# Optimization experiments

Measured on AMD Instinct MI355X. Metric: run time of the kernel, lower is better.

Reference implementation:

```python
import jax, jax.numpy as jnp
import numpy as np

# Config constants (mirror EnergyConfig)
MIN_CARD = 26.0
CARD_PEN = 25.0
PLANE_W = 1.0
FACET_W = 8.0
RANK_EPS = 1e-6
BOUND_W = 4.0
SUP_W = 1.0
ACT_W = 1.0
INACT_W = 0.35
MARGIN = 0.05
PROB_POW = 1.0
PLANE_TOPK = 128
ACTIVE_TOPK = 64

N_POINTS, DIM, BATCH = 65536, 8, 256


def _topk_filter(w, k):
    # Keep only the top-k entries per row, zero elsewhere (scatter of gathered values).
    if k <= 0 or k >= w.shape[-1]:
        return w
    vals, idx = jax.lax.top_k(w, k)
    rows = jnp.arange(w.shape[0])[:, None]
    return jnp.zeros_like(w).at[rows, idx].set(vals)


def setup_inputs() -> dict:
    key = jax.random.key(0)
    k1, k2 = jax.random.split(key)
    probabilities = jax.random.uniform(k1, (BATCH, N_POINTS), dtype=jnp.float32)
    points = jax.random.normal(k2, (N_POINTS, DIM), dtype=jnp.float32)
    return {"probabilities": probabilities, "points": points}


def reference(probabilities, points):
    prob = jnp.clip(probabilities, 1e-5, 1.0 - 1e-5)  # (B,N)

    # ---- weighted plane statistics (weighted PCA) ----
    pw = _topk_filter(prob, PLANE_TOPK)                       # (B,N)
    wsum = jnp.clip(pw.sum(-1), 1e-6)                          # (B,)
    mean = (pw @ points) / wsum[:, None]                       # (B,D)
    pp = points[:, :, None] * points[:, None, :]               # (N,D,D), small since D=8
    second_moment = jnp.einsum('bn,nij->bij', pw, pp) / wsum[:, None, None]
    cov = second_moment - mean[:, :, None] * mean[:, None, :]  # (B,D,D)
    cov = 0.5 * (cov + cov.swapaxes(1, 2))
    eigvals, eigvecs = jnp.linalg.eigh(cov)                    # ascending
    plane_term = eigvals[:, 0]
    second_eig = eigvals[:, 1]
    facet_term = plane_term / (second_eig + RANK_EPS)
    normal = eigvecs[:, :, 0]                                  # (B,D) smallest-eig direction

    # ---- dual-orientation boundary terms ----
    proj = points @ normal.T                                   # (N,B)
    active_w = _topk_filter(prob ** PROB_POW, ACTIVE_TOPK)     # (B,N)
    active_norm = jnp.clip(active_w.sum(-1), 1e-6)
    inactive_w = 1.0 - prob
    inactive_norm = jnp.clip(inactive_w.sum(-1), 1e-6)

    def orientation_boundary(p):
        # p: (N,B) oriented projections
        offset = -p.max(axis=0)                                # (B,)
        signed = p + offset[None, :]                           # (N,B), max is 0
        sb = signed.T                                          # (B,N)
        active_res = sb * sb                                   # quadratic active loss
        active = (active_w * active_res).sum(-1) / active_norm
        slack = jax.nn.relu(MARGIN + sb)
        inactive = (inactive_w * slack * slack).sum(-1) / inactive_norm
        support = jax.nn.relu(signed.max(axis=0)) ** 2
        return SUP_W * support + ACT_W * active + INACT_W * inactive

    b_pos = orientation_boundary(proj)
    b_neg = orientation_boundary(-proj)
    boundary = jnp.where(b_pos <= b_neg, b_pos, b_neg)

    # ---- cardinality penalty ----
    cardinality = prob.sum(-1)
    deficit = jax.nn.relu(MIN_CARD - cardinality)
    card_term = CARD_PEN * deficit * deficit

    total = PLANE_W * plane_term + FACET_W * facet_term + BOUND_W * boundary + card_term
    return total
```

## Files before the change

kernel.cpp:

```cpp
#include <hip/hip_runtime.h>
#include <cstdint>
#include <cstddef>

constexpr int NPTS   = 65536;
constexpr int B      = 256;
constexpr int CHUNKS = 8;
constexpr int CHUNK  = NPTS / CHUNKS;
constexpr int CCAP   = 160;
constexpr int NBLK   = B * CHUNKS;
constexpr int NEARCAP = 256;

constexpr size_t WSO_CBUF    = 0;
constexpr size_t WSO_NEAR    = WSO_CBUF + (size_t)NBLK * CCAP * 2;
constexpr size_t WSO_NEARCNT = WSO_NEAR + (size_t)2 * B * NEARCAP * 2;
constexpr size_t WSO_PSUM    = WSO_NEARCNT + 2 * B;
constexpr size_t WSO_CCNT    = WSO_PSUM + NBLK;
constexpr size_t WSO_PLANE   = WSO_CCNT + NBLK;
constexpr size_t WSO_FACET   = WSO_PLANE + B;
constexpr size_t WSO_NRM     = WSO_FACET + B;
constexpr size_t WSO_SUMP    = WSO_NRM + (size_t)B * 8;
constexpr size_t WSO_ANORM   = WSO_SUMP + B;
constexpr size_t WSO_T64V    = WSO_ANORM + B;
constexpr size_t WSO_T64I    = WSO_T64V + (size_t)B * 64;
constexpr size_t WSO_PMAXP   = WSO_T64I + (size_t)B * 64;
constexpr size_t WSO_PMAXN   = WSO_PMAXP + B;

constexpr int PPB = 64;
constexpr int NPB = NPTS / PPB;
constexpr size_t WSO_PART = WSO_CBUF;

__device__ __forceinline__ float clipp(float x) {
    return fminf(fmaxf(x, 1e-5f), 0.99999f);
}
__device__ __forceinline__ unsigned f2mono(float f) {
    unsigned u = __float_as_uint(f);
    return (u & 0x80000000u) ? ~u : (u | 0x80000000u);
}
__device__ __forceinline__ float mono2f(unsigned e) {
    return __uint_as_float((e & 0x80000000u) ? (e ^ 0x80000000u) : ~e);
}
__device__ __forceinline__ int cand_bin(float v) {
    int b = (int)((v - 0.99f) * 102400.0f);
    return min(max(b, 0), 1023);
}
__device__ __forceinline__ float dot8(float4 a, float4 b, const float* n) {
    float d = a.x * n[0];
    d = fmaf(a.y, n[1], d); d = fmaf(a.z, n[2], d); d = fmaf(a.w, n[3], d);
    d = fmaf(b.x, n[4], d); d = fmaf(b.y, n[5], d); d = fmaf(b.z, n[6], d);
    d = fmaf(b.w, n[7], d);
    return d;
}
__device__ __forceinline__ float dot8v(float4 a, float4 b, float4 n0, float4 n1) {
    float d = a.x * n0.x;
    d = fmaf(a.y, n0.y, d); d = fmaf(a.z, n0.z, d); d = fmaf(a.w, n0.w, d);
    d = fmaf(b.x, n1.x, d); d = fmaf(b.y, n1.y, d); d = fmaf(b.z, n1.z, d);
    d = fmaf(b.w, n1.w, d);
    return d;
}

__global__ __launch_bounds__(256) void kA_stream(
    const float* __restrict__ prob, float* __restrict__ ws)
{
    __shared__ float wred[4];
    __shared__ int lcnt;
    const int tid   = threadIdx.x;
    const int row   = blockIdx.x >> 3;
    const int chunk = blockIdx.x & 7;
    if (tid == 0) lcnt = 0;
    __syncthreads();

    unsigned long long* cb = (unsigned long long*)ws + (size_t)blockIdx.x * CCAP;
    const float4* p4 = (const float4*)(prob + (size_t)row * NPTS + (size_t)chunk * CHUNK);

    float4 v[8];
    #pragma unroll
    for (int i = 0; i < 8; i++) v[i] = p4[i * 256 + tid];

    float lsum = 0.f;
    #pragma unroll
    for (int i = 0; i < 8; i++) {
        float c0 = clipp(v[i].x), c1 = clipp(v[i].y), c2 = clipp(v[i].z), c3 = clipp(v[i].w);
        lsum += (c0 + c1) + (c2 + c3);
        float mx = fmaxf(fmaxf(c0, c1), fmaxf(c2, c3));
        if (mx >= 0.99f) {
            int bi = chunk * CHUNK + (i * 256 + tid) * 4;
            float c4[4] = {c0, c1, c2, c3};
            #pragma unroll
            for (int j = 0; j < 4; j++) {
                if (c4[j] >= 0.99f) {
                    int p_ = atomicAdd(&lcnt, 1);
                    if (p_ < CCAP)
                        cb[p_] = (((unsigned long long)__float_as_uint(c4[j])) << 32)
                               | (unsigned)~(bi + j);
                }
            }
        }
    }
    #pragma unroll
    for (int off = 32; off; off >>= 1) lsum += __shfl_down(lsum, off);
    if ((tid & 63) == 0) wred[tid >> 6] = lsum;
    __syncthreads();
    if (tid == 0) {
        ws[WSO_PSUM + blockIdx.x] = (wred[0] + wred[1]) + (wred[2] + wred[3]);
        ((int*)ws)[WSO_CCNT + blockIdx.x] = min(lcnt, CCAP);
    }
}

constexpr int CSLOTS = CHUNKS * CCAP;
constexpr int GITER  = CSLOTS / 256;
__global__ __launch_bounds__(256) void kB_select(
    const float* __restrict__ points, float* __restrict__ ws)
{
    __shared__ unsigned long long cand[CSLOTS];
    __shared__ unsigned long long comp[256];
    __shared__ int   hist[1024];
    __shared__ int   counts_s[CHUNKS];
    __shared__ int   ccnt_s, bt_s;
    __shared__ float sw[128];
    __shared__ float pc[128][9];
    __shared__ float sred[44][4];
    __shared__ float slotm[44];
    __shared__ float wpart[2];
    __shared__ float covm[64];

    const int row = blockIdx.x;
    const int tid = threadIdx.x;

    if (tid < CHUNKS) counts_s[tid] = ((const int*)ws)[WSO_CCNT + row * CHUNKS + tid];
    if (tid == 0) { ccnt_s = 0; bt_s = 0; }
    #pragma unroll
    for (int k = 0; k < 4; k++) hist[tid * 4 + k] = 0;
    __syncthreads();

    const unsigned long long* cb = (const unsigned long long*)ws;
    #pragma unroll
    for (int r = 0; r < GITER; r++) {
        int s = r * 256 + tid;
        int c = s / CCAP, t = s - c * CCAP;
        unsigned long long k = 0ull;
        if (t < counts_s[c]) {
            k = cb[(size_t)(row * CHUNKS + c) * CCAP + t];
            atomicAdd(&hist[cand_bin(__uint_as_float((unsigned)(k >> 32)))], 1);
        }
        cand[s] = k;
    }
    __syncthreads();

    if (tid < 64) {
        int h[16]; int g = 0;
        #pragma unroll
        for (int k = 0; k < 16; k++) { h[k] = hist[tid * 16 + k]; g += h[k]; }
        int s = g;
        #pragma unroll
        for (int off = 1; off < 64; off <<= 1) {
            int o = __shfl_down(s, off);
            if (tid + off < 64) s += o;
        }
        int Snext = __shfl_down(s, 1);
        if (tid == 63) Snext = 0;
        if (s >= 128 && Snext < 128) {
            int acc = Snext, bt = tid * 16;
            #pragma unroll
            for (int k = 15; k >= 0; k--) {
                acc += h[k];
                if (acc >= 128) { bt = tid * 16 + k; break; }
            }
            bt_s = bt;
        }
    }
    __syncthreads();

    const int bt = bt_s;
    #pragma unroll
    for (int r = 0; r < GITER; r++) {
        unsigned long long k = cand[r * 256 + tid];
        if (k && cand_bin(__uint_as_float((unsigned)(k >> 32))) >= bt) {
            int p_ = atomicAdd(&ccnt_s, 1);
            if (p_ < 256) comp[p_] = k;
        }
    }
    __syncthreads();
    const int m = min(ccnt_s, 256);

    if (tid < 128) {
        sw[tid] = 0.f;
        #pragma unroll
        for (int j = 0; j < 9; j++) pc[tid][j] = (j == 8) ? 1.f : 0.f;
    }
    if (tid < 64) {
        ws[WSO_T64V + (size_t)row * 64 + tid] = 0.f;
        ((int*)ws)[WSO_T64I + (size_t)row * 64 + tid] = 0;
    }
    unsigned long long ki = (tid < m) ? comp[tid] : 0ull;
    int rank = 0;
    for (int j = 0; j < m; j++) rank += (comp[j] > ki) ? 1 : 0;
    __syncthreads();

    if (tid < m && rank < 128) {
        float v = __uint_as_float((unsigned)(ki >> 32));
        unsigned idx = ~(unsigned)(ki & 0xFFFFFFFFu);
        sw[rank] = v;
        const float4* pt = (const float4*)(points + (size_t)idx * 8);
        float4 q0 = pt[0], q1 = pt[1];
        pc[rank][0] = q0.x; pc[rank][1] = q0.y; pc[rank][2] = q0.z; pc[rank][3] = q0.w;
        pc[rank][4] = q1.x; pc[rank][5] = q1.y; pc[rank][6] = q1.z; pc[rank][7] = q1.w;
        if (rank < 64) {
            ws[WSO_T64V + (size_t)row * 64 + rank] = v;
            ((int*)ws)[WSO_T64I + (size_t)row * 64 + rank] = (int)idx;
        }
    }
    __syncthreads();

    if (tid < 128) {
        float ww = sw[tid];
        #pragma unroll
        for (int off = 32; off; off >>= 1) ww += __shfl_down(ww, off);
        if ((tid & 63) == 0) wpart[tid >> 6] = ww;
    }
    if (tid < 176) {
        int s = tid >> 2, part = tid & 3;
        int i_, j_;
        if (s < 36) {
            int rem = s; i_ = 0;
            while (rem >= 8 - i_) { rem -= 8 - i_; i_++; }
            j_ = i_ + rem;
        } else { i_ = s - 36; j_ = 8; }
        float acc = 0.f;
        for (int k = part * 32; k < part * 32 + 32; k++)
            acc += sw[k] * pc[k][i_] * pc[k][j_];
        sred[s][part] = acc;
    }
    __syncthreads();
    if (tid < 44) slotm[tid] = (sred[tid][0] + sred[tid][1]) + (sred[tid][2] + sred[tid][3]);
    __syncthreads();

    if (tid < 64) {
        float w128 = fmaxf(wpart[0] + wpart[1], 1e-6f);
        int i_ = tid >> 3, j_ = tid & 7;
        int a_ = min(i_, j_), b_ = max(i_, j_);
        int s3 = 8 * a_ - (a_ * (a_ - 1)) / 2 + (b_ - a_);
        covm[tid] = slotm[s3] / w128 - (slotm[36 + i_] / w128) * (slotm[36 + j_] / w128);
    }
    __syncthreads();

    if (tid == 64) {
        ws[WSO_ANORM + row] = fmaxf(wpart[0], 1e-6f);
        float s = 0.f;
        for (int c = 0; c < CHUNKS; c++) s += ws[WSO_PSUM + row * CHUNKS + c];
        ws[WSO_SUMP + row] = s;
        ((unsigned*)ws)[WSO_PMAXP + row] = 0u;
        ((unsigned*)ws)[WSO_PMAXN + row] = 0u;
        ((int*)ws)[WSO_NEARCNT + row * 2 + 0] = 0;
        ((int*)ws)[WSO_NEARCNT + row * 2 + 1] = 0;
    }

    if (tid < 64) {
        const int i = tid >> 3, j = tid & 7;
        float a = covm[tid];
        float v = (i == j) ? 1.f : 0.f;
        const unsigned PR[7] = {023456701u, 001234567u, 050712346u, 034067125u,
                                012305674u, 067120453u, 045671032u};
        #pragma unroll 1
        for (int sweep = 0; sweep < 6; sweep++) {
            #pragma unroll
            for (int r = 0; r < 7; r++) {
                const unsigned pk = PR[r];
                const int rp = (pk >> (3 * i)) & 7;
                const int cp = (pk >> (3 * j)) & 7;
                const int pr = min(i, rp), qr = max(i, rp);
                float app = __shfl(a, pr * 9);
                float aqq = __shfl(a, qr * 9);
                float apq = __shfl(a, pr * 8 + qr);
                float tau = 0.5f * (aqq - app);
                float den = fabsf(tau) + sqrtf(fmaf(tau, tau, apq * apq));
                float t = __fdividef(apq, den + 1e-38f);
                t = (tau < 0.f) ? -t : t;
                float cr = rsqrtf(fmaf(t, t, 1.f));
                float sr = t * cr;
                float cc = __shfl(cr, j * 9);
                float sc = __shfl(sr, j * 9);
                float oth = __shfl(a, rp * 8 + j);
                a = fmaf((i < rp) ? -sr : sr, oth, cr * a);
                float oth2 = __shfl(a, i * 8 + cp);
                a = fmaf((j < cp) ? -sc : sc, oth2, cc * a);
                float ov = __shfl(v, i * 8 + cp);
                v = fmaf((j < cp) ? -sc : sc, ov, cc * v);
            }
        }
        float d[8];
        #pragma unroll
        for (int k = 0; k < 8; k++) d[k] = __shfl(a, k * 9);
        float e0 = d[0]; int i0 = 0;
        #pragma unroll
        for (int k = 1; k < 8; k++) if (d[k] < e0) { e0 = d[k]; i0 = k; }
        float e1 = 3.4e38f;
        #pragma unroll
        for (int k = 0; k < 8; k++) if (k != i0 && d[k] < e1) e1 = d[k];
        if (tid == 0) {
            ws[WSO_PLANE + row] = e0;
            ws[WSO_FACET + row] = e0 / (e1 + 1e-6f);
        }
        if (j == i0) ws[WSO_NRM + (size_t)row * 8 + i] = v;
    }
}

__global__ __launch_bounds__(256) void k3a_max(
    const float* __restrict__ points, float* __restrict__ ws)
{
    const int t  = threadIdx.x;
    const int pb = blockIdx.x;
    const float4* nv = (const float4*)(ws + WSO_NRM);
    float4 n0 = nv[t * 2], n1 = nv[t * 2 + 1];
    const float4* pq = (const float4*)points + (size_t)pb * (PPB * 2);
    float mp = -3.4e38f, mn = -3.4e38f;
    #pragma unroll 8
    for (int i = 0; i < PPB; i++) {
        float4 a = pq[2 * i], b = pq[2 * i + 1];
        float d = dot8v(a, b, n0, n1);
        mp = fmaxf(mp, d);
        mn = fmaxf(mn, -d);
    }
    float* part = ws + WSO_PART + (size_t)pb * 512;
    part[t * 2]     = mp;
    part[t * 2 + 1] = mn;
}

__global__ __launch_bounds__(256) void k3r_reduce(float* __restrict__ ws)
{
    const int tg = blockIdx.x * 256 + threadIdx.x;
    const int rs = tg & 511;
    const int g  = tg >> 9;
    const float* part = ws + WSO_PART;
    float m = -3.4e38f;
    #pragma unroll 8
    for (int i = 0; i < NPB / 8; i++)
        m = fmaxf(m, part[(size_t)(g * (NPB / 8) + i) * 512 + rs]);
    unsigned* wsu = (unsigned*)ws;
    atomicMax(&wsu[((rs & 1) ? WSO_PMAXN : WSO_PMAXP) + (rs >> 1)], f2mono(m));
}

__global__ __launch_bounds__(256) void k3b_near(
    const float* __restrict__ points, float* __restrict__ ws)
{
    const int t  = threadIdx.x;
    const int pb = blockIdx.x;
    const unsigned* wsu = (const unsigned*)ws;
    const float4* nv = (const float4*)(ws + WSO_NRM);
    float4 n0 = nv[t * 2], n1 = nv[t * 2 + 1];
    const float thp = mono2f(wsu[WSO_PMAXP + t]) - 0.05f;
    const float thn = mono2f(wsu[WSO_PMAXN + t]) - 0.05f;
    const float4* pq = (const float4*)points + (size_t)pb * (PPB * 2);
    int* ncnt = (int*)ws + WSO_NEARCNT;
    unsigned long long* nbuf = (unsigned long long*)ws + WSO_NEAR / 2;
    #pragma unroll 4
    for (int i = 0; i < PPB; i++) {
        float4 a = pq[2 * i], b = pq[2 * i + 1];
        float d = dot8v(a, b, n0, n1);
        int nidx = pb * PPB + i;
        if (d >= thp) {
            int p_ = atomicAdd(&ncnt[t * 2 + 0], 1);
            if (p_ < NEARCAP)
                nbuf[(size_t)(t * 2 + 0) * NEARCAP + p_] =
                    (((unsigned long long)__float_as_uint(d)) << 32) | (unsigned)nidx;
        }
        if (-d >= thn) {
            int p_ = atomicAdd(&ncnt[t * 2 + 1], 1);
            if (p_ < NEARCAP)
                nbuf[(size_t)(t * 2 + 1) * NEARCAP + p_] =
                    (((unsigned long long)__float_as_uint(-d)) << 32) | (unsigned)nidx;
        }
    }
}

__global__ __launch_bounds__(64) void k3cd_final(
    const float* __restrict__ points, const float* __restrict__ prob,
    const float* __restrict__ ws, float* __restrict__ out)
{
    const int row = blockIdx.x;
    const int t   = threadIdx.x;
    const unsigned* wsu = (const unsigned*)ws;
    __shared__ float nl[8];
    if (t < 8) nl[t] = ws[WSO_NRM + (size_t)row * 8 + t];
    __syncthreads();

    const float pmaxp = mono2f(wsu[WSO_PMAXP + row]);
    const float pmaxn = mono2f(wsu[WSO_PMAXN + row]);

    float w   = ws[WSO_T64V + (size_t)row * 64 + t];
    int   idx = ((const int*)ws)[WSO_T64I + (size_t)row * 64 + t];
    const float4* pt = (const float4*)(points + (size_t)idx * 8);
    float4 q0 = pt[0], q1 = pt[1];
    float d = dot8(q0, q1, nl);
    float sp = d - pmaxp, sn = -d - pmaxn;
    float ap = w * sp * sp;
    float an = w * sn * sn;

    const int* ncnt = (const int*)ws + WSO_NEARCNT;
    const unsigned long long* nbuf = (const unsigned long long*)ws + WSO_NEAR / 2;
    float ip = 0.f, in_ = 0.f;
    int cp = min(ncnt[row * 2 + 0], NEARCAP);
    int cn = min(ncnt[row * 2 + 1], NEARCAP);
    for (int i = t; i < cp; i += 64) {
        unsigned long long e = nbuf[(size_t)(row * 2 + 0) * NEARCAP + i];
        float dv = __uint_as_float((unsigned)(e >> 32));
        float tp = 0.05f + (dv - pmaxp);
        if (tp > 0.f) {
            float w2 = 1.0f - clipp(prob[(size_t)row * NPTS + (unsigned)(e & 0xFFFFFFFFu)]);
            ip = fmaf(w2 * tp, tp, ip);
        }
    }
    for (int i = t; i < cn; i += 64) {
        unsigned long long e = nbuf[(size_t)(row * 2 + 1) * NEARCAP + i];
        float dv = __uint_as_float((unsigned)(e >> 32));
        float tn = 0.05f + (dv - pmaxn);
        if (tn > 0.f) {
            float w2 = 1.0f - clipp(prob[(size_t)row * NPTS + (unsigned)(e & 0xFFFFFFFFu)]);
            in_ = fmaf(w2 * tn, tn, in_);
        }
    }
    #pragma unroll
    for (int off = 32; off; off >>= 1) {
        ap  += __shfl_down(ap, off);
        an  += __shfl_down(an, off);
        ip  += __shfl_down(ip, off);
        in_ += __shfl_down(in_, off);
    }
    if (t == 0) {
        float anorm = ws[WSO_ANORM + row];
        float sump  = ws[WSO_SUMP + row];
        float inorm = fmaxf((float)NPTS - sump, 1e-6f);
        float bp = (ap / anorm) + 0.35f * (ip / inorm);
        float bn = (an / anorm) + 0.35f * (in_ / inorm);
        float bd = (bp <= bn) ? bp : bn;
        float def = fmaxf(26.0f - sump, 0.f);
        out[row] = ws[WSO_PLANE + row] + 8.0f * ws[WSO_FACET + row]
                 + 4.0f * bd + 25.0f * def * def;
    }
}

extern "C" void kernel_launch(void* const* d_in, const int* in_sizes, int n_in,
                              void* d_out, int out_size, void* d_ws, size_t ws_size,
                              hipStream_t stream) {
    const float* prob   = (const float*)d_in[0];
    const float* points = (const float*)d_in[1];
    float* out = (float*)d_out;
    float* ws  = (float*)d_ws;

    kA_stream<<<NBLK, 256, 0, stream>>>(prob, ws);
    kB_select<<<B, 256, 0, stream>>>(points, ws);
    k3a_max<<<NPB, 256, 0, stream>>>(points, ws);
    k3r_reduce<<<16, 256, 0, stream>>>(ws);
    k3b_near<<<NPB, 256, 0, stream>>>(points, ws);
    k3cd_final<<<B, 64, 0, stream>>>(points, prob, ws, out);
}
```

Measured before the change: 154.1 us.

## Fuse all stages into one persistent kernel with software grid barriers

Replaces six kernel launches with a single persistent kernel of one 512-thread block per row. Blocks synchronize through an atomic generation-counter grid barrier, and candidate buffers, top-64 lists and plane statistics move from global workspace into shared memory. The near-boundary stage now accumulates the inactive loss directly with atomics instead of collecting candidate lists, and a memset zeroes the barrier and accumulators. This removes launch gaps and workspace round-trips, but it relies on all 256 blocks being co-resident, and each row's prob pass now runs on a single block.

```diff
diff --git a/kernel.cpp b/kernel.cpp
--- a/kernel.cpp
+++ b/kernel.cpp
@@ -2,32 +2,18 @@
 #include <cstdint>
 #include <cstddef>
 
-constexpr int NPTS   = 65536;
-constexpr int B      = 256;
-constexpr int CHUNKS = 8;
-constexpr int CHUNK  = NPTS / CHUNKS;
-constexpr int CCAP   = 160;
-constexpr int NBLK   = B * CHUNKS;
-constexpr int NEARCAP = 256;
-
-constexpr size_t WSO_CBUF    = 0;
-constexpr size_t WSO_NEAR    = WSO_CBUF + (size_t)NBLK * CCAP * 2;
-constexpr size_t WSO_NEARCNT = WSO_NEAR + (size_t)2 * B * NEARCAP * 2;
-constexpr size_t WSO_PSUM    = WSO_NEARCNT + 2 * B;
-constexpr size_t WSO_CCNT    = WSO_PSUM + NBLK;
-constexpr size_t WSO_PLANE   = WSO_CCNT + NBLK;
-constexpr size_t WSO_FACET   = WSO_PLANE + B;
-constexpr size_t WSO_NRM     = WSO_FACET + B;
-constexpr size_t WSO_SUMP    = WSO_NRM + (size_t)B * 8;
-constexpr size_t WSO_ANORM   = WSO_SUMP + B;
-constexpr size_t WSO_T64V    = WSO_ANORM + B;
-constexpr size_t WSO_T64I    = WSO_T64V + (size_t)B * 64;
-constexpr size_t WSO_PMAXP   = WSO_T64I + (size_t)B * 64;
-constexpr size_t WSO_PMAXN   = WSO_PMAXP + B;
-
-constexpr int PPB = 64;
-constexpr int NPB = NPTS / PPB;
-constexpr size_t WSO_PART = WSO_CBUF;
+constexpr int NPTS = 65536;
+constexpr int B    = 256;
+constexpr int TPB  = 512;
+constexpr int CCAND = 1024;
+
+constexpr size_t WSO_BAR   = 0;
+constexpr size_t WSO_PMAXP = 4;
+constexpr size_t WSO_PMAXN = 260;
+constexpr size_t WSO_ISUMP = 516;
+constexpr size_t WSO_ISUMN = 772;
+constexpr size_t WSO_INIT_WORDS = 1028;
+constexpr size_t WSO_NRM   = 1028;
 
 __device__ __forceinline__ float clipp(float x) {
     return fminf(fmaxf(x, 1e-5f), 0.99999f);
@@ -42,13 +28,6 @@
 __device__ __forceinline__ int cand_bin(float v) {
     int b = (int)((v - 0.99f) * 102400.0f);
     return min(max(b, 0), 1023);
-}
-__device__ __forceinline__ float dot8(float4 a, float4 b, const float* n) {
-    float d = a.x * n[0];
-    d = fmaf(a.y, n[1], d); d = fmaf(a.z, n[2], d); d = fmaf(a.w, n[3], d);
-    d = fmaf(b.x, n[4], d); d = fmaf(b.y, n[5], d); d = fmaf(b.z, n[6], d);
-    d = fmaf(b.w, n[7], d);
-    return d;
 }
 __device__ __forceinline__ float dot8v(float4 a, float4 b, float4 n0, float4 n1) {
     float d = a.x * n0.x;
@@ -58,99 +37,111 @@
     return d;
 }
 
-__global__ __launch_bounds__(256) void kA_stream(
-    const float* __restrict__ prob, float* __restrict__ ws)
+__device__ __forceinline__ void gridbar(unsigned* bar, unsigned nblk) {
+    __syncthreads();
+    if (threadIdx.x == 0) {
+        __threadfence();
+        unsigned old = __hip_atomic_fetch_add(bar, 1u, __ATOMIC_ACQ_REL,
+                                              __HIP_MEMORY_SCOPE_AGENT);
+        unsigned mygen = old >> 16;
+        if ((old & 0xFFFFu) == nblk - 1u) {
+            __hip_atomic_fetch_add(bar, (1u << 16) - nblk, __ATOMIC_ACQ_REL,
+                                   __HIP_MEMORY_SCOPE_AGENT);
+        } else {
+            int guard = 0;
+            while ((__hip_atomic_load(bar, __ATOMIC_ACQUIRE,
+                                      __HIP_MEMORY_SCOPE_AGENT) >> 16) == mygen) {
+                __builtin_amdgcn_s_sleep(32);
+                if (++guard > (1 << 22)) break;
+            }
+        }
+        __threadfence();
+    }
+    __syncthreads();
+}
+
+__global__ __launch_bounds__(TPB) void kFused(
+    const float* __restrict__ prob, const float* __restrict__ points,
+    float* __restrict__ ws, float* __restrict__ out)
 {
-    __shared__ float wred[4];
-    __shared__ int lcnt;
-    const int tid   = threadIdx.x;
-    const int row   = blockIdx.x >> 3;
-    const int chunk = blockIdx.x & 7;
-    if (tid == 0) lcnt = 0;
-    __syncthreads();
-
-    unsigned long long* cb = (unsigned long long*)ws + (size_t)blockIdx.x * CCAP;
-    const float4* p4 = (const float4*)(prob + (size_t)row * NPTS + (size_t)chunk * CHUNK);
-
-    float4 v[8];
-    #pragma unroll
-    for (int i = 0; i < 8; i++) v[i] = p4[i * 256 + tid];
-
-    float lsum = 0.f;
-    #pragma unroll
-    for (int i = 0; i < 8; i++) {
-        float c0 = clipp(v[i].x), c1 = clipp(v[i].y), c2 = clipp(v[i].z), c3 = clipp(v[i].w);
-        lsum += (c0 + c1) + (c2 + c3);
-        float mx = fmaxf(fmaxf(c0, c1), fmaxf(c2, c3));
-        if (mx >= 0.99f) {
-            int bi = chunk * CHUNK + (i * 256 + tid) * 4;
-            float c4[4] = {c0, c1, c2, c3};
-            #pragma unroll
-            for (int j = 0; j < 4; j++) {
-                if (c4[j] >= 0.99f) {
-                    int p_ = atomicAdd(&lcnt, 1);
-                    if (p_ < CCAP)
-                        cb[p_] = (((unsigned long long)__float_as_uint(c4[j])) << 32)
-                               | (unsigned)~(bi + j);
-                }
-            }
-        }
-    }
-    #pragma unroll
-    for (int off = 32; off; off >>= 1) lsum += __shfl_down(lsum, off);
-    if ((tid & 63) == 0) wred[tid >> 6] = lsum;
-    __syncthreads();
-    if (tid == 0) {
-        ws[WSO_PSUM + blockIdx.x] = (wred[0] + wred[1]) + (wred[2] + wred[3]);
-        ((int*)ws)[WSO_CCNT + blockIdx.x] = min(lcnt, CCAP);
-    }
-}
-
-constexpr int CSLOTS = CHUNKS * CCAP;
-constexpr int GITER  = CSLOTS / 256;
-__global__ __launch_bounds__(256) void kB_select(
-    const float* __restrict__ points, float* __restrict__ ws)
-{
-    __shared__ unsigned long long cand[CSLOTS];
+    __shared__ __align__(16) unsigned long long cand[CCAND];
     __shared__ unsigned long long comp[256];
     __shared__ int   hist[1024];
-    __shared__ int   counts_s[CHUNKS];
-    __shared__ int   ccnt_s, bt_s;
     __shared__ float sw[128];
     __shared__ float pc[128][9];
     __shared__ float sred[44][4];
     __shared__ float slotm[44];
     __shared__ float wpart[2];
     __shared__ float covm[64];
-
+    __shared__ float t64v[64];
+    __shared__ int   t64i[64];
+    __shared__ __align__(16) float nrm_s[8];
+    __shared__ float wred8[8];
+    __shared__ float plane_s, facet_s, anorm_s, sump_s;
+    __shared__ int   lcnt, ccnt, bt_s;
+
+    const int tid = threadIdx.x;
     const int row = blockIdx.x;
-    const int tid = threadIdx.x;
-
-    if (tid < CHUNKS) counts_s[tid] = ((const int*)ws)[WSO_CCNT + row * CHUNKS + tid];
-    if (tid == 0) { ccnt_s = 0; bt_s = 0; }
-    #pragma unroll
-    for (int k = 0; k < 4; k++) hist[tid * 4 + k] = 0;
-    __syncthreads();
-
-    const unsigned long long* cb = (const unsigned long long*)ws;
-    #pragma unroll
-    for (int r = 0; r < GITER; r++) {
-        int s = r * 256 + tid;
-        int c = s / CCAP, t = s - c * CCAP;
-        unsigned long long k = 0ull;
-        if (t < counts_s[c]) {
-            k = cb[(size_t)(row * CHUNKS + c) * CCAP + t];
-            atomicAdd(&hist[cand_bin(__uint_as_float((unsigned)(k >> 32)))], 1);
-        }
-        cand[s] = k;
-    }
+    float* nrm_all = (float*)cand;
+    float* maxf    = (float*)hist;
+    unsigned* bar  = (unsigned*)ws + WSO_BAR;
+
+    hist[tid] = 0; hist[tid + 512] = 0;
+    if (tid == 0) { lcnt = 0; ccnt = 0; bt_s = 0; }
+    __syncthreads();
+
+    {
+        const float4* p4 = (const float4*)(prob + (size_t)row * NPTS);
+        float lsum = 0.f;
+        #pragma unroll 1
+        for (int g = 0; g < 4; g++) {
+            float4 v[8];
+            #pragma unroll
+            for (int i = 0; i < 8; i++) v[i] = p4[(g * 8 + i) * TPB + tid];
+            #pragma unroll
+            for (int i = 0; i < 8; i++) {
+                float c0 = clipp(v[i].x), c1 = clipp(v[i].y);
+                float c2 = clipp(v[i].z), c3 = clipp(v[i].w);
+                lsum += (c0 + c1) + (c2 + c3);
+                float mx = fmaxf(fmaxf(c0, c1), fmaxf(c2, c3));
+                if (mx >= 0.99f) {
+                    int bi = ((g * 8 + i) * TPB + tid) * 4;
+                    float c4[4] = {c0, c1, c2, c3};
+                    #pragma unroll
+                    for (int j = 0; j < 4; j++) {
+                        if (c4[j] >= 0.99f) {
+                            int p_ = atomicAdd(&lcnt, 1);
+                            if (p_ < CCAND)
+                                cand[p_] = (((unsigned long long)__float_as_uint(c4[j])) << 32)
+                                         | (unsigned)~(bi + j);
+                        }
+                    }
+                }
+            }
+        }
+        #pragma unroll
+        for (int off = 32; off; off >>= 1) lsum += __shfl_down(lsum, off);
+        if ((tid & 63) == 0) wred8[tid >> 6] = lsum;
+    }
+    __syncthreads();
+    if (tid == 0) {
+        float s = 0.f;
+        #pragma unroll
+        for (int k = 0; k < 8; k++) s += wred8[k];
+        sump_s = s;
+    }
+    __syncthreads();
+
+    const int mc = min(lcnt, CCAND);
+    for (int i = tid; i < mc; i += TPB)
+        atomicAdd(&hist[cand_bin(__uint_as_float((unsigned)(cand[i] >> 32)))], 1);
     __syncthreads();
 
     if (tid < 64) {
-        int h[16]; int g = 0;
-        #pragma unroll
-        for (int k = 0; k < 16; k++) { h[k] = hist[tid * 16 + k]; g += h[k]; }
-        int s = g;
+        int h[16]; int g2 = 0;
+        #pragma unroll
+        for (int k = 0; k < 16; k++) { h[k] = hist[tid * 16 + k]; g2 += h[k]; }
+        int s = g2;
         #pragma unroll
         for (int off = 1; off < 64; off <<= 1) {
             int o = __shfl_down(s, off);
@@ -170,27 +161,23 @@
     }
     __syncthreads();
 
-    const int bt = bt_s;
-    #pragma unroll
-    for (int r = 0; r < GITER; r++) {
-        unsigned long long k = cand[r * 256 + tid];
-        if (k && cand_bin(__uint_as_float((unsigned)(k >> 32))) >= bt) {
-            int p_ = atomicAdd(&ccnt_s, 1);
+    const int btv = bt_s;
+    for (int i = tid; i < mc; i += TPB) {
+        unsigned long long k = cand[i];
+        if (cand_bin(__uint_as_float((unsigned)(k >> 32))) >= btv) {
+            int p_ = atomicAdd(&ccnt, 1);
             if (p_ < 256) comp[p_] = k;
         }
     }
     __syncthreads();
-    const int m = min(ccnt_s, 256);
+    const int m = min(ccnt, 256);
 
     if (tid < 128) {
         sw[tid] = 0.f;
         #pragma unroll
         for (int j = 0; j < 9; j++) pc[tid][j] = (j == 8) ? 1.f : 0.f;
     }
-    if (tid < 64) {
-        ws[WSO_T64V + (size_t)row * 64 + tid] = 0.f;
-        ((int*)ws)[WSO_T64I + (size_t)row * 64 + tid] = 0;
-    }
+    if (tid < 64) { t64v[tid] = 0.f; t64i[tid] = 0; }
     unsigned long long ki = (tid < m) ? comp[tid] : 0ull;
     int rank = 0;
     for (int j = 0; j < m; j++) rank += (comp[j] > ki) ? 1 : 0;
@@ -204,10 +191,7 @@
         float4 q0 = pt[0], q1 = pt[1];
         pc[rank][0] = q0.x; pc[rank][1] = q0.y; pc[rank][2] = q0.z; pc[rank][3] = q0.w;
         pc[rank][4] = q1.x; pc[rank][5] = q1.y; pc[rank][6] = q1.z; pc[rank][7] = q1.w;
-        if (rank < 64) {
-            ws[WSO_T64V + (size_t)row * 64 + rank] = v;
-            ((int*)ws)[WSO_T64I + (size_t)row * 64 + rank] = (int)idx;
-        }
+        if (rank < 64) { t64v[rank] = v; t64i[rank] = (int)idx; }
     }
     __syncthreads();
 
@@ -241,18 +225,8 @@
         int s3 = 8 * a_ - (a_ * (a_ - 1)) / 2 + (b_ - a_);
         covm[tid] = slotm[s3] / w128 - (slotm[36 + i_] / w128) * (slotm[36 + j_] / w128);
     }
-    __syncthreads();
-
-    if (tid == 64) {
-        ws[WSO_ANORM + row] = fmaxf(wpart[0], 1e-6f);
-        float s = 0.f;
-        for (int c = 0; c < CHUNKS; c++) s += ws[WSO_PSUM + row * CHUNKS + c];
-        ws[WSO_SUMP + row] = s;
-        ((unsigned*)ws)[WSO_PMAXP + row] = 0u;
-        ((unsigned*)ws)[WSO_PMAXN + row] = 0u;
-        ((int*)ws)[WSO_NEARCNT + row * 2 + 0] = 0;
-        ((int*)ws)[WSO_NEARCNT + row * 2 + 1] = 0;
-    }
+    if (tid == 64) anorm_s = fmaxf(wpart[0], 1e-6f);
+    __syncthreads();
 
     if (tid < 64) {
         const int i = tid >> 3, j = tid & 7;
@@ -287,154 +261,112 @@
                 v = fmaf((j < cp) ? -sc : sc, ov, cc * v);
             }
         }
-        float d[8];
-        #pragma unroll
-        for (int k = 0; k < 8; k++) d[k] = __shfl(a, k * 9);
-        float e0 = d[0]; int i0 = 0;
-        #pragma unroll
-        for (int k = 1; k < 8; k++) if (d[k] < e0) { e0 = d[k]; i0 = k; }
+        float dd[8];
+        #pragma unroll
+        for (int k = 0; k < 8; k++) dd[k] = __shfl(a, k * 9);
+        float e0 = dd[0]; int i0 = 0;
+        #pragma unroll
+        for (int k = 1; k < 8; k++) if (dd[k] < e0) { e0 = dd[k]; i0 = k; }
         float e1 = 3.4e38f;
         #pragma unroll
-        for (int k = 0; k < 8; k++) if (k != i0 && d[k] < e1) e1 = d[k];
+        for (int k = 0; k < 8; k++) if (k != i0 && dd[k] < e1) e1 = dd[k];
+        if (tid == 0) { plane_s = e0; facet_s = e0 / (e1 + 1e-6f); }
+        if (j == i0) { nrm_s[i] = v; ws[WSO_NRM + (size_t)row * 8 + i] = v; }
+    }
+
+    gridbar(bar, gridDim.x);
+
+    ((float4*)nrm_all)[tid] = ((const float4*)(ws + WSO_NRM))[tid];
+    __syncthreads();
+    const int rt = tid & 255, sub = tid >> 8;
+    const float4 n0 = ((float4*)nrm_all)[rt * 2], n1 = ((float4*)nrm_all)[rt * 2 + 1];
+    const float4* pq = (const float4*)points
+                     + ((size_t)blockIdx.x * 256 + (size_t)sub * 128) * 2;
+    {
+        float mp = -3.4e38f, mn = -3.4e38f;
+        #pragma unroll 8
+        for (int i = 0; i < 128; i++) {
+            float4 a = pq[2 * i], b = pq[2 * i + 1];
+            float d = dot8v(a, b, n0, n1);
+            mp = fmaxf(mp, d);
+            mn = fmaxf(mn, -d);
+        }
+        maxf[tid] = mp; maxf[512 + tid] = mn;
+    }
+    __syncthreads();
+    if (tid < 256) {
+        float mpf = fmaxf(maxf[tid], maxf[tid + 256]);
+        float mnf = fmaxf(maxf[512 + tid], maxf[512 + tid + 256]);
+        unsigned* wsu = (unsigned*)ws;
+        atomicMax(&wsu[WSO_PMAXP + tid], f2mono(mpf));
+        atomicMax(&wsu[WSO_PMAXN + tid], f2mono(mnf));
+    }
+
+    gridbar(bar, gridDim.x);
+
+    if (tid < 256) {
+        unsigned* wsu = (unsigned*)ws;
+        maxf[tid] = mono2f(__hip_atomic_load(&wsu[WSO_PMAXP + tid],
+                            __ATOMIC_ACQUIRE, __HIP_MEMORY_SCOPE_AGENT));
+        maxf[256 + tid] = mono2f(__hip_atomic_load(&wsu[WSO_PMAXN + tid],
+                            __ATOMIC_ACQUIRE, __HIP_MEMORY_SCOPE_AGENT));
+    }
+    __syncthreads();
+    {
+        const float pvp = maxf[rt], pvn = maxf[256 + rt];
+        const int gbase = blockIdx.x * 256 + sub * 128;
+        float accp = 0.f, accn = 0.f;
+        #pragma unroll 4
+        for (int i = 0; i < 128; i++) {
+            float4 a = pq[2 * i], b = pq[2 * i + 1];
+            float d = dot8v(a, b, n0, n1);
+            float tp = 0.05f + (d - pvp);
+            float tn = 0.05f + (-d - pvn);
+            if (tp > 0.f || tn > 0.f) {
+                float w2 = 1.0f - clipp(prob[(size_t)rt * NPTS + (gbase + i)]);
+                if (tp > 0.f) accp = fmaf(w2 * tp, tp, accp);
+                if (tn > 0.f) accn = fmaf(w2 * tn, tn, accn);
+            }
+        }
+        if (accp != 0.f) atomicAdd(ws + WSO_ISUMP + rt, accp);
+        if (accn != 0.f) atomicAdd(ws + WSO_ISUMN + rt, accn);
+    }
+
+    gridbar(bar, gridDim.x);
+
+    if (tid < 64) {
+        unsigned* wsu = (unsigned*)ws;
+        float pmaxp = mono2f(__hip_atomic_load(&wsu[WSO_PMAXP + row],
+                              __ATOMIC_ACQUIRE, __HIP_MEMORY_SCOPE_AGENT));
+        float pmaxn = mono2f(__hip_atomic_load(&wsu[WSO_PMAXN + row],
+                              __ATOMIC_ACQUIRE, __HIP_MEMORY_SCOPE_AGENT));
+        float4 m0 = *(const float4*)&nrm_s[0];
+        float4 m1 = *(const float4*)&nrm_s[4];
+        float w   = t64v[tid];
+        int   idx = t64i[tid];
+        const float4* pt = (const float4*)(points + (size_t)idx * 8);
+        float4 q0 = pt[0], q1 = pt[1];
+        float d = dot8v(q0, q1, m0, m1);
+        float sp = d - pmaxp, sn = -d - pmaxn;
+        float ap = w * sp * sp;
+        float an = w * sn * sn;
+        #pragma unroll
+        for (int off = 32; off; off >>= 1) {
+            ap += __shfl_down(ap, off);
+            an += __shfl_down(an, off);
+        }
         if (tid == 0) {
-            ws[WSO_PLANE + row] = e0;
-            ws[WSO_FACET + row] = e0 / (e1 + 1e-6f);
-        }
-        if (j == i0) ws[WSO_NRM + (size_t)row * 8 + i] = v;
-    }
-}
-
-__global__ __launch_bounds__(256) void k3a_max(
-    const float* __restrict__ points, float* __restrict__ ws)
-{
-    const int t  = threadIdx.x;
-    const int pb = blockIdx.x;
-    const float4* nv = (const float4*)(ws + WSO_NRM);
-    float4 n0 = nv[t * 2], n1 = nv[t * 2 + 1];
-    const float4* pq = (const float4*)points + (size_t)pb * (PPB * 2);
-    float mp = -3.4e38f, mn = -3.4e38f;
-    #pragma unroll 8
-    for (int i = 0; i < PPB; i++) {
-        float4 a = pq[2 * i], b = pq[2 * i + 1];
-        float d = dot8v(a, b, n0, n1);
-        mp = fmaxf(mp, d);
-        mn = fmaxf(mn, -d);
-    }
-    float* part = ws + WSO_PART + (size_t)pb * 512;
-    part[t * 2]     = mp;
-    part[t * 2 + 1] = mn;
-}
-
-__global__ __launch_bounds__(256) void k3r_reduce(float* __restrict__ ws)
-{
-    const int tg = blockIdx.x * 256 + threadIdx.x;
-    const int rs = tg & 511;
-    const int g  = tg >> 9;
-    const float* part = ws + WSO_PART;
-    float m = -3.4e38f;
-    #pragma unroll 8
-    for (int i = 0; i < NPB / 8; i++)
-        m = fmaxf(m, part[(size_t)(g * (NPB / 8) + i) * 512 + rs]);
-    unsigned* wsu = (unsigned*)ws;
-    atomicMax(&wsu[((rs & 1) ? WSO_PMAXN : WSO_PMAXP) + (rs >> 1)], f2mono(m));
-}
-
-__global__ __launch_bounds__(256) void k3b_near(
-    const float* __restrict__ points, float* __restrict__ ws)
-{
-    const int t  = threadIdx.x;
-    const int pb = blockIdx.x;
-    const unsigned* wsu = (const unsigned*)ws;
-    const float4* nv = (const float4*)(ws + WSO_NRM);
-    float4 n0 = nv[t * 2], n1 = nv[t * 2 + 1];
-    const float thp = mono2f(wsu[WSO_PMAXP + t]) - 0.05f;
-    const float thn = mono2f(wsu[WSO_PMAXN + t]) - 0.05f;
-    const float4* pq = (const float4*)points + (size_t)pb * (PPB * 2);
-    int* ncnt = (int*)ws + WSO_NEARCNT;
-    unsigned long long* nbuf = (unsigned long long*)ws + WSO_NEAR / 2;
-    #pragma unroll 4
-    for (int i = 0; i < PPB; i++) {
-        float4 a = pq[2 * i], b = pq[2 * i + 1];
-        float d = dot8v(a, b, n0, n1);
-        int nidx = pb * PPB + i;
-        if (d >= thp) {
-            int p_ = atomicAdd(&ncnt[t * 2 + 0], 1);
-            if (p_ < NEARCAP)
-                nbuf[(size_t)(t * 2 + 0) * NEARCAP + p_] =
-                    (((unsigned long long)__float_as_uint(d)) << 32) | (unsigned)nidx;
-        }
-        if (-d >= thn) {
-            int p_ = atomicAdd(&ncnt[t * 2 + 1], 1);
-            if (p_ < NEARCAP)
-                nbuf[(size_t)(t * 2 + 1) * NEARCAP + p_] =
-                    (((unsigned long long)__float_as_uint(-d)) << 32) | (unsigned)nidx;
-        }
-    }
-}
-
-__global__ __launch_bounds__(64) void k3cd_final(
-    const float* __restrict__ points, const float* __restrict__ prob,
-    const float* __restrict__ ws, float* __restrict__ out)
-{
-    const int row = blockIdx.x;
-    const int t   = threadIdx.x;
-    const unsigned* wsu = (const unsigned*)ws;
-    __shared__ float nl[8];
-    if (t < 8) nl[t] = ws[WSO_NRM + (size_t)row * 8 + t];
-    __syncthreads();
-
-    const float pmaxp = mono2f(wsu[WSO_PMAXP + row]);
-    const float pmaxn = mono2f(wsu[WSO_PMAXN + row]);
-
-    float w   = ws[WSO_T64V + (size_t)row * 64 + t];
-    int   idx = ((const int*)ws)[WSO_T64I + (size_t)row * 64 + t];
-    const float4* pt = (const float4*)(points + (size_t)idx * 8);
-    float4 q0 = pt[0], q1 = pt[1];
-    float d = dot8(q0, q1, nl);
-    float sp = d - pmaxp, sn = -d - pmaxn;
-    float ap = w * sp * sp;
-    float an = w * sn * sn;
-
-    const int* ncnt = (const int*)ws + WSO_NEARCNT;
-    const unsigned long long* nbuf = (const unsigned long long*)ws + WSO_NEAR / 2;
-    float ip = 0.f, in_ = 0.f;
-    int cp = min(ncnt[row * 2 + 0], NEARCAP);
-    int cn = min(ncnt[row * 2 + 1], NEARCAP);
-    for (int i = t; i < cp; i += 64) {
-        unsigned long long e = nbuf[(size_t)(row * 2 + 0) * NEARCAP + i];
-        float dv = __uint_as_float((unsigned)(e >> 32));
-        float tp = 0.05f + (dv - pmaxp);
-        if (tp > 0.f) {
-            float w2 = 1.0f - clipp(prob[(size_t)row * NPTS + (unsigned)(e & 0xFFFFFFFFu)]);
-            ip = fmaf(w2 * tp, tp, ip);
-        }
-    }
-    for (int i = t; i < cn; i += 64) {
-        unsigned long long e = nbuf[(size_t)(row * 2 + 1) * NEARCAP + i];
-        float dv = __uint_as_float((unsigned)(e >> 32));
-        float tn = 0.05f + (dv - pmaxn);
-        if (tn > 0.f) {
-            float w2 = 1.0f - clipp(prob[(size_t)row * NPTS + (unsigned)(e & 0xFFFFFFFFu)]);
-            in_ = fmaf(w2 * tn, tn, in_);
-        }
-    }
-    #pragma unroll
-    for (int off = 32; off; off >>= 1) {
-        ap  += __shfl_down(ap, off);
-        an  += __shfl_down(an, off);
-        ip  += __shfl_down(ip, off);
-        in_ += __shfl_down(in_, off);
-    }
-    if (t == 0) {
-        float anorm = ws[WSO_ANORM + row];
-        float sump  = ws[WSO_SUMP + row];
-        float inorm = fmaxf((float)NPTS - sump, 1e-6f);
-        float bp = (ap / anorm) + 0.35f * (ip / inorm);
-        float bn = (an / anorm) + 0.35f * (in_ / inorm);
-        float bd = (bp <= bn) ? bp : bn;
-        float def = fmaxf(26.0f - sump, 0.f);
-        out[row] = ws[WSO_PLANE + row] + 8.0f * ws[WSO_FACET + row]
-                 + 4.0f * bd + 25.0f * def * def;
+            float ip  = __hip_atomic_load(ws + WSO_ISUMP + row,
+                          __ATOMIC_ACQUIRE, __HIP_MEMORY_SCOPE_AGENT);
+            float in_ = __hip_atomic_load(ws + WSO_ISUMN + row,
+                          __ATOMIC_ACQUIRE, __HIP_MEMORY_SCOPE_AGENT);
+            float inorm = fmaxf((float)NPTS - sump_s, 1e-6f);
+            float bp = (ap / anorm_s) + 0.35f * (ip / inorm);
+            float bn = (an / anorm_s) + 0.35f * (in_ / inorm);
+            float bd = (bp <= bn) ? bp : bn;
+            float def = fmaxf(26.0f - sump_s, 0.f);
+            out[row] = plane_s + 8.0f * facet_s + 4.0f * bd + 25.0f * def * def;
+        }
     }
 }
 
@@ -446,10 +378,6 @@
     float* out = (float*)d_out;
     float* ws  = (float*)d_ws;
 
-    kA_stream<<<NBLK, 256, 0, stream>>>(prob, ws);
-    kB_select<<<B, 256, 0, stream>>>(points, ws);
-    k3a_max<<<NPB, 256, 0, stream>>>(points, ws);
-    k3r_reduce<<<16, 256, 0, stream>>>(ws);
-    k3b_near<<<NPB, 256, 0, stream>>>(points, ws);
-    k3cd_final<<<B, 64, 0, stream>>>(points, prob, ws, out);
-}
+    hipMemsetAsync(ws, 0, WSO_INIT_WORDS * sizeof(float), stream);
+    kFused<<<B, TPB, 0, stream>>>(prob, points, ws, out);
+}
```

Measured after the change: 247.4 us. 1.61x slower.

## Fuse max reduce and final kernels via last-block pattern, drop near-list

Applied to the files above, without the earlier changes.

Replaces the separate max-reduce kernel with a last-block-done reduction inside the max kernel. Removes the near-candidate list and final per-row kernel: the inactive term is accumulated directly per point/row with atomics, and the last block computes active terms and the output. Points are staged in shared memory. This cuts two launches but makes the inactive pass read prob at strided addresses for near points, and the single last block serially scans all partials, a serial tail.

```diff
diff --git a/kernel.cpp b/kernel.cpp
--- a/kernel.cpp
+++ b/kernel.cpp
@@ -8,47 +8,32 @@
 constexpr int CHUNK  = NPTS / CHUNKS;
 constexpr int CCAP   = 160;
 constexpr int NBLK   = B * CHUNKS;
-constexpr int NEARCAP = 256;
-
-constexpr size_t WSO_CBUF    = 0;
-constexpr size_t WSO_NEAR    = WSO_CBUF + (size_t)NBLK * CCAP * 2;
-constexpr size_t WSO_NEARCNT = WSO_NEAR + (size_t)2 * B * NEARCAP * 2;
-constexpr size_t WSO_PSUM    = WSO_NEARCNT + 2 * B;
-constexpr size_t WSO_CCNT    = WSO_PSUM + NBLK;
-constexpr size_t WSO_PLANE   = WSO_CCNT + NBLK;
-constexpr size_t WSO_FACET   = WSO_PLANE + B;
-constexpr size_t WSO_NRM     = WSO_FACET + B;
-constexpr size_t WSO_SUMP    = WSO_NRM + (size_t)B * 8;
-constexpr size_t WSO_ANORM   = WSO_SUMP + B;
-constexpr size_t WSO_T64V    = WSO_ANORM + B;
-constexpr size_t WSO_T64I    = WSO_T64V + (size_t)B * 64;
-constexpr size_t WSO_PMAXP   = WSO_T64I + (size_t)B * 64;
-constexpr size_t WSO_PMAXN   = WSO_PMAXP + B;
-
-constexpr int PPB = 64;
-constexpr int NPB = NPTS / PPB;
-constexpr size_t WSO_PART = WSO_CBUF;
+constexpr int PPB    = 64;
+constexpr int NPB    = NPTS / PPB;
+
+constexpr size_t WSO_CBUF  = 0;
+constexpr size_t WSO_PART  = 0;
+constexpr size_t WSO_PSUM  = 655360;
+constexpr size_t WSO_CCNT  = WSO_PSUM + NBLK;
+constexpr size_t WSO_PLANE = WSO_CCNT + NBLK;
+constexpr size_t WSO_FACET = WSO_PLANE + B;
+constexpr size_t WSO_NRM   = WSO_FACET + B;
+constexpr size_t WSO_SUMP  = WSO_NRM + (size_t)B * 8;
+constexpr size_t WSO_ANORM = WSO_SUMP + B;
+constexpr size_t WSO_T64V  = WSO_ANORM + B;
+constexpr size_t WSO_T64I  = WSO_T64V + (size_t)B * 64;
+constexpr size_t WSO_PMAXP = WSO_T64I + (size_t)B * 64;
+constexpr size_t WSO_PMAXN = WSO_PMAXP + B;
+constexpr size_t WSO_ISUMP = WSO_PMAXN + B;
+constexpr size_t WSO_ISUMN = WSO_ISUMP + B;
+constexpr size_t WSO_CNT   = WSO_ISUMN + B;
 
 __device__ __forceinline__ float clipp(float x) {
     return fminf(fmaxf(x, 1e-5f), 0.99999f);
-}
-__device__ __forceinline__ unsigned f2mono(float f) {
-    unsigned u = __float_as_uint(f);
-    return (u & 0x80000000u) ? ~u : (u | 0x80000000u);
-}
-__device__ __forceinline__ float mono2f(unsigned e) {
-    return __uint_as_float((e & 0x80000000u) ? (e ^ 0x80000000u) : ~e);
 }
 __device__ __forceinline__ int cand_bin(float v) {
     int b = (int)((v - 0.99f) * 102400.0f);
     return min(max(b, 0), 1023);
-}
-__device__ __forceinline__ float dot8(float4 a, float4 b, const float* n) {
-    float d = a.x * n[0];
-    d = fmaf(a.y, n[1], d); d = fmaf(a.z, n[2], d); d = fmaf(a.w, n[3], d);
-    d = fmaf(b.x, n[4], d); d = fmaf(b.y, n[5], d); d = fmaf(b.z, n[6], d);
-    d = fmaf(b.w, n[7], d);
-    return d;
 }
 __device__ __forceinline__ float dot8v(float4 a, float4 b, float4 n0, float4 n1) {
     float d = a.x * n0.x;
@@ -248,10 +233,14 @@
         float s = 0.f;
         for (int c = 0; c < CHUNKS; c++) s += ws[WSO_PSUM + row * CHUNKS + c];
         ws[WSO_SUMP + row] = s;
-        ((unsigned*)ws)[WSO_PMAXP + row] = 0u;
-        ((unsigned*)ws)[WSO_PMAXN + row] = 0u;
-        ((int*)ws)[WSO_NEARCNT + row * 2 + 0] = 0;
-        ((int*)ws)[WSO_NEARCNT + row * 2 + 1] = 0;
+    }
+    if (tid == 127 && row == 0) {
+        ((unsigned*)ws)[WSO_CNT + 0] = 0u;
+        ((unsigned*)ws)[WSO_CNT + 1] = 0u;
+    }
+    if (tid >= 128 && row < 2) {
+        ws[WSO_ISUMP + (size_t)row * 256 + (tid - 128) * 2 + 0] = 0.f;
+        ws[WSO_ISUMP + (size_t)row * 256 + (tid - 128) * 2 + 1] = 0.f;
     }
 
     if (tid < 64) {
@@ -307,133 +296,113 @@
 __global__ __launch_bounds__(256) void k3a_max(
     const float* __restrict__ points, float* __restrict__ ws)
 {
-    const int t  = threadIdx.x;
-    const int pb = blockIdx.x;
+    __shared__ __align__(16) float pts[PPB * 8];
+    __shared__ int lastflag;
+    const int tid = threadIdx.x;
+    const int pb  = blockIdx.x;
+    if (tid < 128) ((float4*)pts)[tid] = ((const float4*)points)[pb * 128 + tid];
+    if (tid == 0) lastflag = 0;
+    __syncthreads();
+
     const float4* nv = (const float4*)(ws + WSO_NRM);
-    float4 n0 = nv[t * 2], n1 = nv[t * 2 + 1];
-    const float4* pq = (const float4*)points + (size_t)pb * (PPB * 2);
+    const float4 n0 = nv[tid * 2], n1 = nv[tid * 2 + 1];
     float mp = -3.4e38f, mn = -3.4e38f;
     #pragma unroll 8
     for (int i = 0; i < PPB; i++) {
-        float4 a = pq[2 * i], b = pq[2 * i + 1];
+        float4 a = ((float4*)pts)[i * 2], b = ((float4*)pts)[i * 2 + 1];
         float d = dot8v(a, b, n0, n1);
         mp = fmaxf(mp, d);
         mn = fmaxf(mn, -d);
     }
-    float* part = ws + WSO_PART + (size_t)pb * 512;
-    part[t * 2]     = mp;
-    part[t * 2 + 1] = mn;
-}
-
-__global__ __launch_bounds__(256) void k3r_reduce(float* __restrict__ ws)
+    ws[WSO_PART + (size_t)pb * 512 + tid * 2 + 0] = mp;
+    ws[WSO_PART + (size_t)pb * 512 + tid * 2 + 1] = mn;
+    __threadfence();
+    __syncthreads();
+    if (tid == 0) {
+        unsigned old = __hip_atomic_fetch_add((unsigned*)ws + WSO_CNT + 0, 1u,
+                                              __ATOMIC_ACQ_REL, __HIP_MEMORY_SCOPE_AGENT);
+        if (old == NPB - 1) lastflag = 1;
+    }
+    __syncthreads();
+    if (lastflag) {
+        __threadfence();
+        const float* part = ws + WSO_PART;
+        float fp = -3.4e38f, fn = -3.4e38f;
+        #pragma unroll 8
+        for (int q = 0; q < NPB; q++) {
+            fp = fmaxf(fp, part[(size_t)q * 512 + tid * 2 + 0]);
+            fn = fmaxf(fn, part[(size_t)q * 512 + tid * 2 + 1]);
+        }
+        ws[WSO_PMAXP + tid] = fp;
+        ws[WSO_PMAXN + tid] = fn;
+    }
+}
+
+__global__ __launch_bounds__(256) void k3b_inact(
+    const float* __restrict__ points, const float* __restrict__ prob,
+    float* __restrict__ ws, float* __restrict__ out)
 {
-    const int tg = blockIdx.x * 256 + threadIdx.x;
-    const int rs = tg & 511;
-    const int g  = tg >> 9;
-    const float* part = ws + WSO_PART;
-    float m = -3.4e38f;
-    #pragma unroll 8
-    for (int i = 0; i < NPB / 8; i++)
-        m = fmaxf(m, part[(size_t)(g * (NPB / 8) + i) * 512 + rs]);
-    unsigned* wsu = (unsigned*)ws;
-    atomicMax(&wsu[((rs & 1) ? WSO_PMAXN : WSO_PMAXP) + (rs >> 1)], f2mono(m));
-}
-
-__global__ __launch_bounds__(256) void k3b_near(
-    const float* __restrict__ points, float* __restrict__ ws)
-{
-    const int t  = threadIdx.x;
-    const int pb = blockIdx.x;
-    const unsigned* wsu = (const unsigned*)ws;
+    __shared__ __align__(16) float pts[PPB * 8];
+    __shared__ int lastflag;
+    const int tid = threadIdx.x;
+    const int pb  = blockIdx.x;
+    if (tid < 128) ((float4*)pts)[tid] = ((const float4*)points)[pb * 128 + tid];
+    if (tid == 0) lastflag = 0;
+    __syncthreads();
+
     const float4* nv = (const float4*)(ws + WSO_NRM);
-    float4 n0 = nv[t * 2], n1 = nv[t * 2 + 1];
-    const float thp = mono2f(wsu[WSO_PMAXP + t]) - 0.05f;
-    const float thn = mono2f(wsu[WSO_PMAXN + t]) - 0.05f;
-    const float4* pq = (const float4*)points + (size_t)pb * (PPB * 2);
-    int* ncnt = (int*)ws + WSO_NEARCNT;
-    unsigned long long* nbuf = (unsigned long long*)ws + WSO_NEAR / 2;
+    const float4 n0 = nv[tid * 2], n1 = nv[tid * 2 + 1];
+    const float pmaxp = ws[WSO_PMAXP + tid];
+    const float pmaxn = ws[WSO_PMAXN + tid];
+    float accp = 0.f, accn = 0.f;
     #pragma unroll 4
     for (int i = 0; i < PPB; i++) {
-        float4 a = pq[2 * i], b = pq[2 * i + 1];
+        float4 a = ((float4*)pts)[i * 2], b = ((float4*)pts)[i * 2 + 1];
         float d = dot8v(a, b, n0, n1);
-        int nidx = pb * PPB + i;
-        if (d >= thp) {
-            int p_ = atomicAdd(&ncnt[t * 2 + 0], 1);
-            if (p_ < NEARCAP)
-                nbuf[(size_t)(t * 2 + 0) * NEARCAP + p_] =
-                    (((unsigned long long)__float_as_uint(d)) << 32) | (unsigned)nidx;
-        }
-        if (-d >= thn) {
-            int p_ = atomicAdd(&ncnt[t * 2 + 1], 1);
-            if (p_ < NEARCAP)
-                nbuf[(size_t)(t * 2 + 1) * NEARCAP + p_] =
-                    (((unsigned long long)__float_as_uint(-d)) << 32) | (unsigned)nidx;
-        }
-    }
-}
-
-__global__ __launch_bounds__(64) void k3cd_final(
-    const float* __restrict__ points, const float* __restrict__ prob,
-    const float* __restrict__ ws, float* __restrict__ out)
-{
-    const int row = blockIdx.x;
-    const int t   = threadIdx.x;
-    const unsigned* wsu = (const unsigned*)ws;
-    __shared__ float nl[8];
-    if (t < 8) nl[t] = ws[WSO_NRM + (size_t)row * 8 + t];
-    __syncthreads();
-
-    const float pmaxp = mono2f(wsu[WSO_PMAXP + row]);
-    const float pmaxn = mono2f(wsu[WSO_PMAXN + row]);
-
-    float w   = ws[WSO_T64V + (size_t)row * 64 + t];
-    int   idx = ((const int*)ws)[WSO_T64I + (size_t)row * 64 + t];
-    const float4* pt = (const float4*)(points + (size_t)idx * 8);
-    float4 q0 = pt[0], q1 = pt[1];
-    float d = dot8(q0, q1, nl);
-    float sp = d - pmaxp, sn = -d - pmaxn;
-    float ap = w * sp * sp;
-    float an = w * sn * sn;
-
-    const int* ncnt = (const int*)ws + WSO_NEARCNT;
-    const unsigned long long* nbuf = (const unsigned long long*)ws + WSO_NEAR / 2;
-    float ip = 0.f, in_ = 0.f;
-    int cp = min(ncnt[row * 2 + 0], NEARCAP);
-    int cn = min(ncnt[row * 2 + 1], NEARCAP);
-    for (int i = t; i < cp; i += 64) {
-        unsigned long long e = nbuf[(size_t)(row * 2 + 0) * NEARCAP + i];
-        float dv = __uint_as_float((unsigned)(e >> 32));
-        float tp = 0.05f + (dv - pmaxp);
-        if (tp > 0.f) {
-            float w2 = 1.0f - clipp(prob[(size_t)row * NPTS + (unsigned)(e & 0xFFFFFFFFu)]);
-            ip = fmaf(w2 * tp, tp, ip);
-        }
-    }
-    for (int i = t; i < cn; i += 64) {
-        unsigned long long e = nbuf[(size_t)(row * 2 + 1) * NEARCAP + i];
-        float dv = __uint_as_float((unsigned)(e >> 32));
-        float tn = 0.05f + (dv - pmaxn);
-        if (tn > 0.f) {
-            float w2 = 1.0f - clipp(prob[(size_t)row * NPTS + (unsigned)(e & 0xFFFFFFFFu)]);
-            in_ = fmaf(w2 * tn, tn, in_);
-        }
-    }
-    #pragma unroll
-    for (int off = 32; off; off >>= 1) {
-        ap  += __shfl_down(ap, off);
-        an  += __shfl_down(an, off);
-        ip  += __shfl_down(ip, off);
-        in_ += __shfl_down(in_, off);
-    }
-    if (t == 0) {
-        float anorm = ws[WSO_ANORM + row];
-        float sump  = ws[WSO_SUMP + row];
+        float tp = 0.05f + (d - pmaxp);
+        float tn = 0.05f + (-d - pmaxn);
+        if (tp > 0.f || tn > 0.f) {
+            float w2 = 1.0f - clipp(prob[(size_t)tid * NPTS + (pb * PPB + i)]);
+            if (tp > 0.f) accp = fmaf(w2 * tp, tp, accp);
+            if (tn > 0.f) accn = fmaf(w2 * tn, tn, accn);
+        }
+    }
+    if (accp != 0.f) atomicAdd(ws + WSO_ISUMP + tid, accp);
+    if (accn != 0.f) atomicAdd(ws + WSO_ISUMN + tid, accn);
+    __threadfence();
+    __syncthreads();
+    if (tid == 0) {
+        unsigned old = __hip_atomic_fetch_add((unsigned*)ws + WSO_CNT + 1, 1u,
+                                              __ATOMIC_ACQ_REL, __HIP_MEMORY_SCOPE_AGENT);
+        if (old == NPB - 1) lastflag = 1;
+    }
+    __syncthreads();
+    if (lastflag) {
+        __threadfence();
+        float ap = 0.f, an = 0.f;
+        #pragma unroll 4
+        for (int i = 0; i < 64; i++) {
+            float w  = ws[WSO_T64V + (size_t)tid * 64 + i];
+            int  idx = ((const int*)ws)[WSO_T64I + (size_t)tid * 64 + i];
+            const float4* pt = (const float4*)(points + (size_t)idx * 8);
+            float4 q0 = pt[0], q1 = pt[1];
+            float d = dot8v(q0, q1, n0, n1);
+            float sp = d - pmaxp, sn = -d - pmaxn;
+            ap = fmaf(w * sp, sp, ap);
+            an = fmaf(w * sn, sn, an);
+        }
+        float ip  = __hip_atomic_load(ws + WSO_ISUMP + tid, __ATOMIC_RELAXED,
+                                      __HIP_MEMORY_SCOPE_AGENT);
+        float in_ = __hip_atomic_load(ws + WSO_ISUMN + tid, __ATOMIC_RELAXED,
+                                      __HIP_MEMORY_SCOPE_AGENT);
+        float anorm = ws[WSO_ANORM + tid];
+        float sump  = ws[WSO_SUMP + tid];
         float inorm = fmaxf((float)NPTS - sump, 1e-6f);
         float bp = (ap / anorm) + 0.35f * (ip / inorm);
         float bn = (an / anorm) + 0.35f * (in_ / inorm);
         float bd = (bp <= bn) ? bp : bn;
         float def = fmaxf(26.0f - sump, 0.f);
-        out[row] = ws[WSO_PLANE + row] + 8.0f * ws[WSO_FACET + row]
+        out[tid] = ws[WSO_PLANE + tid] + 8.0f * ws[WSO_FACET + tid]
                  + 4.0f * bd + 25.0f * def * def;
     }
 }
@@ -449,7 +418,5 @@
     kA_stream<<<NBLK, 256, 0, stream>>>(prob, ws);
     kB_select<<<B, 256, 0, stream>>>(points, ws);
     k3a_max<<<NPB, 256, 0, stream>>>(points, ws);
-    k3r_reduce<<<16, 256, 0, stream>>>(ws);
-    k3b_near<<<NPB, 256, 0, stream>>>(points, ws);
-    k3cd_final<<<B, 64, 0, stream>>>(points, prob, ws, out);
-}
+    k3b_inact<<<NPB, 256, 0, stream>>>(points, prob, ws, out);
+}
```

After: 372.1 us. +141.4%, slower.
